# Kernel optimization log

Hardware: AMD Instinct MI355X
Metric: run time of the kernel (lower is better)

Reference implementation:

```python
import jax, jax.numpy as jnp
import numpy as np

EPS = 1e-5

def layer_norm(x, gamma, beta):
    mu = jnp.mean(x, axis=-1, keepdims=True)
    var = jnp.mean(jnp.square(x - mu), axis=-1, keepdims=True)
    return (x - mu) * jax.lax.rsqrt(var + EPS) * gamma + beta

def setup_inputs() -> dict:
    key = jax.random.key(0)
    ks = jax.random.split(key, 8)
    B, N, CZ, C = 1, 512, 128, 128
    s_z = 1.0 / np.sqrt(CZ)
    s_c = 1.0 / np.sqrt(C)
    return {
        "pair_rep": jax.random.normal(ks[0], (B, N, N, CZ), dtype=jnp.float32),
        "ln1_gamma": jnp.ones((CZ,), jnp.float32),
        "ln1_beta": jnp.zeros((CZ,), jnp.float32),
        "w_gate_a": jax.random.normal(ks[1], (CZ, C), jnp.float32) * s_z,
        "w_gate_b": jax.random.normal(ks[2], (CZ, C), jnp.float32) * s_z,
        "w_a": jax.random.normal(ks[3], (CZ, C), jnp.float32) * s_z,
        "w_b": jax.random.normal(ks[4], (CZ, C), jnp.float32) * s_z,
        "ln2_gamma": jnp.ones((C,), jnp.float32),
        "ln2_beta": jnp.zeros((C,), jnp.float32),
        "w_out": jax.random.normal(ks[5], (C, CZ), jnp.float32) * s_c,
        "w_gate": jax.random.normal(ks[6], (CZ, CZ), jnp.float32) * s_z,
    }

def reference(pair_rep, ln1_gamma, ln1_beta, w_gate_a, w_gate_b, w_a, w_b,
              ln2_gamma, ln2_beta, w_out, w_gate):
    # pair_rep: [B, N, N, CZ]
    z = layer_norm(pair_rep, ln1_gamma, ln1_beta)
    a = jax.nn.sigmoid(z @ w_gate_a) * (z @ w_a)   # [B, N, N, C]
    b = jax.nn.sigmoid(z @ w_gate_b) * (z @ w_b)   # [B, N, N, C]
    g = jax.nn.sigmoid(z @ w_gate)                 # [B, N, N, CZ]
    # triangle multiplicative update (outgoing): sum over third node k
    upd = jnp.einsum('bikc,bjkc->bijc', a, b)      # [B, N, N, C]
    upd = layer_norm(upd, ln2_gamma, ln2_beta) @ w_out  # [B, N, N, CZ]
    return g * upd
```

## Files before the change

### kernel.cpp

```cpp
#include <hip/hip_runtime.h>

#define N_ 512
#define NPOS (N_*N_)
#define CD 128

typedef unsigned short ushort_t;
typedef unsigned int   uint_t;
typedef __bf16 bf16_t;
typedef bf16_t  bf16x8 __attribute__((ext_vector_type(8)));
typedef float   f32x4  __attribute__((ext_vector_type(4)));
typedef unsigned short u16x4 __attribute__((ext_vector_type(4)));
typedef uint_t  u32x4 __attribute__((ext_vector_type(4)));

__device__ __forceinline__ float bf2f(ushort_t h) {
  union { uint_t u; float f; } v; v.u = ((uint_t)h) << 16; return v.f;
}
__device__ __forceinline__ ushort_t f2bf(float f) {
  union { float f; uint_t u; } v; v.f = f;
  uint_t u = v.u;
  return (ushort_t)((u + 0x7FFFu + ((u >> 16) & 1u)) >> 16);
}
__device__ __forceinline__ float sigm(float x) { return 1.0f / (1.0f + __expf(-x)); }

__global__ void k_tw(const float* s0, const float* s1, const float* s2,
                     const float* s3, const float* s4, const float* s5,
                     ushort_t* dst) {
  const float* s;
  switch (blockIdx.x) {
    case 0: s = s0; break; case 1: s = s1; break; case 2: s = s2; break;
    case 3: s = s3; break; case 4: s = s4; break; default: s = s5; break;
  }
  ushort_t* d = dst + blockIdx.x * CD * CD;
  for (int idx = threadIdx.x; idx < CD * CD; idx += 256) {
    int c = idx >> 7, k = idx & 127;
    d[idx] = f2bf(s[k * CD + c]);
  }
}

__global__ void k_ln1(const float* __restrict__ x, const float* __restrict__ gma,
                      const float* __restrict__ bta, ushort_t* __restrict__ z) {
  int row  = blockIdx.x * 4 + (threadIdx.x >> 6);
  int lane = threadIdx.x & 63;
  float2 pv = ((const float2*)(x + (size_t)row * CD))[lane];
  float x0 = pv.x, x1 = pv.y;
  float s = x0 + x1, q = x0 * x0 + x1 * x1;
  #pragma unroll
  for (int o = 32; o > 0; o >>= 1) { s += __shfl_xor(s, o, 64); q += __shfl_xor(q, o, 64); }
  float mu = s * (1.0f / 128.0f);
  float rs = rsqrtf(q * (1.0f / 128.0f) - mu * mu + 1e-5f);
  float2 gv = ((const float2*)gma)[lane];
  float2 bv = ((const float2*)bta)[lane];
  float z0 = (x0 - mu) * rs * gv.x + bv.x;
  float z1 = (x1 - mu) * rs * gv.y + bv.y;
  ((uint_t*)(z + (size_t)row * CD))[lane] = (uint_t)f2bf(z0) | ((uint_t)f2bf(z1) << 16);
}

__global__ __launch_bounds__(256, 1)
void k_proj(const ushort_t* __restrict__ z, const ushort_t* __restrict__ wT,
            ushort_t* __restrict__ aT, ushort_t* __restrict__ bT,
            float* __restrict__ g) {
  __shared__ ushort_t zl[128 * 128];
  __shared__ ushort_t tb[128][136];
  const int tid = threadIdx.x;
  const int lane = tid & 63, w = tid >> 6;
  const int qd = lane >> 4, l15 = lane & 15;

  bf16x8 wf[5][2][4];
  #pragma unroll
  for (int m = 0; m < 5; ++m)
    #pragma unroll
    for (int i = 0; i < 2; ++i)
      #pragma unroll
      for (int kk = 0; kk < 4; ++kk)
        wf[m][i][kk] = *(const bf16x8*)(wT + m * CD * CD + (w * 32 + i * 16 + l15) * CD + kk * 32 + qd * 8);

  const int TILES = 8;
  const int base = blockIdx.x * TILES;

  u32x4 st[8];
  {
    const u32x4* src = (const u32x4*)(z + (size_t)base * 128 * CD);
    #pragma unroll
    for (int i = 0; i < 8; ++i) st[i] = src[tid + i * 256];
  }

  for (int t = 0; t < TILES; ++t) {
    const int pos0 = (base + t) * 128;
    __syncthreads();
    {
      u32x4* dst = (u32x4*)zl;
      #pragma unroll
      for (int i = 0; i < 8; ++i) {
        int u = tid + i * 256, row = u >> 4;
        dst[(u & ~15) | ((u & 15) ^ (row & 7))] = st[i];
      }
    }
    __syncthreads();
    if (t + 1 < TILES) {
      const u32x4* src = (const u32x4*)(z + (size_t)(base + t + 1) * 128 * CD);
      #pragma unroll
      for (int i = 0; i < 8; ++i) st[i] = src[tid + i * 256];
    }

    #pragma unroll
    for (int ab = 0; ab < 2; ++ab) {
      f32x4 ag[2][8] = {}; f32x4 av[2][8] = {};
      #pragma unroll
      for (int kk = 0; kk < 4; ++kk) {
        bf16x8 zf[8];
        #pragma unroll
        for (int j = 0; j < 8; ++j) {
          int row = j * 16 + l15, kq = kk * 4 + qd;
          zf[j] = ((const bf16x8*)zl)[(row << 4) | (kq ^ (row & 7))];
        }
        #pragma unroll
        for (int j = 0; j < 8; ++j)
          #pragma unroll
          for (int i = 0; i < 2; ++i) {
            ag[i][j] = __builtin_amdgcn_mfma_f32_16x16x32_bf16(wf[ab * 2][i][kk],     zf[j], ag[i][j], 0, 0, 0);
            av[i][j] = __builtin_amdgcn_mfma_f32_16x16x32_bf16(wf[ab * 2 + 1][i][kk], zf[j], av[i][j], 0, 0, 0);
          }
      }
      #pragma unroll
      for (int i = 0; i < 2; ++i)
        #pragma unroll
        for (int j = 0; j < 8; ++j)
          #pragma unroll
          for (int r = 0; r < 4; ++r)
            tb[w * 32 + i * 16 + qd * 4 + r][j * 16 + l15] = f2bf(sigm(ag[i][j][r]) * av[i][j][r]);
      __syncthreads();
      {
        ushort_t* dst = ab ? bT : aT;
        #pragma unroll
        for (int it = 0; it < 8; ++it) {
          int idx = tid + it * 256;
          int row = idx >> 4, c16 = idx & 15;
          u32x4 v = *(const u32x4*)&tb[row][c16 * 8];
          *(u32x4*)&dst[(size_t)row * NPOS + pos0 + c16 * 8] = v;
        }
      }
      __syncthreads();
    }

    {
      f32x4 acc[2][8] = {};
      #pragma unroll
      for (int kk = 0; kk < 4; ++kk) {
        bf16x8 zf[8];
        #pragma unroll
        for (int j = 0; j < 8; ++j) {
          int row = j * 16 + l15, kq = kk * 4 + qd;
          zf[j] = ((const bf16x8*)zl)[(row << 4) | (kq ^ (row & 7))];
        }
        #pragma unroll
        for (int j = 0; j < 8; ++j)
          #pragma unroll
          for (int i = 0; i < 2; ++i)
            acc[i][j] = __builtin_amdgcn_mfma_f32_16x16x32_bf16(wf[4][i][kk], zf[j], acc[i][j], 0, 0, 0);
      }
      #pragma unroll
      for (int i = 0; i < 2; ++i) {
        int cz = w * 32 + i * 16 + qd * 4;
        #pragma unroll
        for (int j = 0; j < 8; ++j) {
          int pos = pos0 + j * 16 + l15;
          float4 pk;
          pk.x = sigm(acc[i][j][0]); pk.y = sigm(acc[i][j][1]);
          pk.z = sigm(acc[i][j][2]); pk.w = sigm(acc[i][j][3]);
          *(float4*)&g[(size_t)pos * CD + cz] = pk;
        }
      }
    }
  }
}

__global__ void k_tri(const ushort_t* __restrict__ aT, const ushort_t* __restrict__ bT,
                      ushort_t* __restrict__ uT) {
  __shared__ ushort_t lA[128][32];
  __shared__ ushort_t lB[128][32];
  __shared__ ushort_t tb[128][136];
  const int tid = threadIdx.x;
  const int lane = tid & 63, wid = tid >> 6;
  const int qd = lane >> 4, l15 = lane & 15;
  const int wm = wid & 1, wn = wid >> 1;
  const int c  = blockIdx.z;
  const int m0 = blockIdx.y * 128, n0 = blockIdx.x * 128;
  const ushort_t* A = aT + (size_t)c * NPOS;
  const ushort_t* B = bT + (size_t)c * NPOS;
  const int sr = tid >> 2, sc = (tid & 3) * 8;
  f32x4 acc[4][4] = {};
  for (int kk = 0; kk < N_; kk += 32) {
    __syncthreads();
    *(u32x4*)&lA[sr     ][sc] = *(const u32x4*)&A[(size_t)(m0 + sr)      * N_ + kk + sc];
    *(u32x4*)&lA[sr + 64][sc] = *(const u32x4*)&A[(size_t)(m0 + 64 + sr) * N_ + kk + sc];
    *(u32x4*)&lB[sr     ][sc] = *(const u32x4*)&B[(size_t)(n0 + sr)      * N_ + kk + sc];
    *(u32x4*)&lB[sr + 64][sc] = *(const u32x4*)&B[(size_t)(n0 + 64 + sr) * N_ + kk + sc];
    __syncthreads();
    bf16x8 af[4], bfr[4];
    #pragma unroll
    for (int t = 0; t < 4; ++t) af[t]  = *(const bf16x8*)&lA[wm * 64 + t * 16 + l15][qd * 8];
    #pragma unroll
    for (int t = 0; t < 4; ++t) bfr[t] = *(const bf16x8*)&lB[wn * 64 + t * 16 + l15][qd * 8];
    #pragma unroll
    for (int i = 0; i < 4; ++i)
      #pragma unroll
      for (int j = 0; j < 4; ++j)
        acc[i][j] = __builtin_amdgcn_mfma_f32_16x16x32_bf16(af[i], bfr[j], acc[i][j], 0, 0, 0);
  }
  #pragma unroll
  for (int i = 0; i < 4; ++i)
    #pragma unroll
    for (int j = 0; j < 4; ++j)
      #pragma unroll
      for (int r2 = 0; r2 < 4; ++r2)
        tb[wm * 64 + i * 16 + qd * 4 + r2][wn * 64 + j * 16 + l15] = f2bf(acc[i][j][r2]);
  __syncthreads();
  ushort_t* U = uT + (size_t)c * NPOS;
  #pragma unroll
  for (int it = 0; it < 8; ++it) {
    int idx = tid + it * 256;
    int row = idx >> 4, c16 = idx & 15;
    u32x4 v = *(const u32x4*)&tb[row][c16 * 8];
    *(u32x4*)&U[(size_t)(m0 + row) * N_ + n0 + c16 * 8] = v;
  }
}

__global__ void k_out(const ushort_t* __restrict__ uT, const ushort_t* __restrict__ wT,
                      const float* __restrict__ g2, const float* __restrict__ b2,
                      float* __restrict__ gout) {
  __shared__ ushort_t nu[128][136];
  __shared__ float ps[2][128], pq[2][128];
  __shared__ float mu[128], rsd[128], gam[128], bet[128];
  const int tid = threadIdx.x;
  const int lane = tid & 63, wid = tid >> 6;
  const int qd = lane >> 4, l15 = lane & 15;
  const int pos0 = blockIdx.x * 128;
  const ushort_t* WoT = wT + 5 * CD * CD;

  if (tid < 128) { gam[tid] = g2[tid]; bet[tid] = b2[tid]; }

  {
    int p = tid & 127, h = tid >> 7;
    float s = 0.f, sq = 0.f;
    for (int cc = h * 64; cc < h * 64 + 64; ++cc) {
      ushort_t raw = uT[(size_t)cc * NPOS + pos0 + p];
      nu[p][cc] = raw;
      float v = bf2f(raw); s += v; sq += v * v;
    }
    ps[h][p] = s; pq[h][p] = sq;
  }
  __syncthreads();
  if (tid < 128) {
    float s = ps[0][tid] + ps[1][tid];
    float m = s * (1.0f / 128.0f);
    float v = (pq[0][tid] + pq[1][tid]) * (1.0f / 128.0f) - m * m;
    mu[tid] = m; rsd[tid] = rsqrtf(v + 1e-5f);
  }
  __syncthreads();
  {
    int p = tid & 127, h = tid >> 7;
    float m = mu[p], rs = rsd[p];
    for (int cc = h * 64; cc < h * 64 + 64; ++cc)
      nu[p][cc] = f2bf((bf2f(nu[p][cc]) - m) * rs * gam[cc] + bet[cc]);
  }
  __syncthreads();

  const int wm = wid & 1, wn = wid >> 1;
  f32x4 acc[4][4] = {};
  for (int kk = 0; kk < 4; ++kk) {
    bf16x8 af[4];
    #pragma unroll
    for (int i = 0; i < 4; ++i)
      af[i] = *(const bf16x8*)(WoT + (wm * 64 + i * 16 + l15) * CD + kk * 32 + qd * 8);
    #pragma unroll
    for (int j = 0; j < 4; ++j) {
      bf16x8 bn = *(const bf16x8*)&nu[wn * 64 + j * 16 + l15][kk * 32 + qd * 8];
      #pragma unroll
      for (int i = 0; i < 4; ++i)
        acc[i][j] = __builtin_amdgcn_mfma_f32_16x16x32_bf16(af[i], bn, acc[i][j], 0, 0, 0);
    }
  }
  #pragma unroll
  for (int i = 0; i < 4; ++i) {
    int cz = wm * 64 + i * 16 + qd * 4;
    #pragma unroll
    for (int j = 0; j < 4; ++j) {
      int pos = pos0 + wn * 64 + j * 16 + l15;
      float4 gv = *(const float4*)&gout[(size_t)pos * CD + cz];
      float4 pk;
      pk.x = gv.x * acc[i][j][0]; pk.y = gv.y * acc[i][j][1];
      pk.z = gv.z * acc[i][j][2]; pk.w = gv.w * acc[i][j][3];
      *(float4*)&gout[(size_t)pos * CD + cz] = pk;
    }
  }
}

extern "C" void kernel_launch(void* const* d_in, const int* in_sizes, int n_in,
                              void* d_out, int out_size, void* d_ws, size_t ws_size,
                              hipStream_t stream) {
  const float* pair = (const float*)d_in[0];
  const float* g1   = (const float*)d_in[1];
  const float* b1   = (const float*)d_in[2];
  const float* wga  = (const float*)d_in[3];
  const float* wgb  = (const float*)d_in[4];
  const float* wa   = (const float*)d_in[5];
  const float* wb   = (const float*)d_in[6];
  const float* g2   = (const float*)d_in[7];
  const float* b2   = (const float*)d_in[8];
  const float* wout = (const float*)d_in[9];
  const float* wg   = (const float*)d_in[10];

  char* ws = (char*)d_ws;
  ushort_t* z  = (ushort_t*)(ws);
  ushort_t* aT = (ushort_t*)(ws + 67108864);
  ushort_t* bT = (ushort_t*)(ws + 134217728);
  ushort_t* wT = (ushort_t*)(ws + 201326592);
  ushort_t* uT = z;
  float*    gb = (float*)d_out;

  k_tw  <<<6, 256, 0, stream>>>(wga, wa, wgb, wb, wg, wout, wT);
  k_ln1 <<<NPOS / 4, 256, 0, stream>>>(pair, g1, b1, z);
  k_proj<<<256, 256, 0, stream>>>(z, wT, aT, bT, gb);
  k_tri <<<dim3(4, 4, 128), 256, 0, stream>>>(aT, bT, uT);
  k_out <<<2048, 256, 0, stream>>>(uT, wT, g2, b2, gb);
}
```

Before: 535.5 us.

## Fuse gate projection into output kernel, double-buffer triangle GEMM, vectorize LN1

The sigmoid gate projection moves from k_proj into k_out. k_out now recomputes LN1 from pair_rep for its 128 positions and runs a second MFMA GEMM against the gate weights alongside the output projection. This removes the 128MB fp32 gate write and its read back through the output buffer, at the cost of re-reading pair_rep and doing extra LDS work. k_tri gains a register-staged, double-buffered LDS pipeline with a swizzled layout, which cuts one barrier per k-step and avoids bank conflicts. k_ln1 is vectorized to 16 lanes per row with float4 loads, and k_proj uses fewer tiles per block with twice as many blocks.

```diff
diff --git a/kernel.cpp b/kernel.cpp
--- a/kernel.cpp
+++ b/kernel.cpp
@@ -39,42 +39,48 @@
 
 __global__ void k_ln1(const float* __restrict__ x, const float* __restrict__ gma,
                       const float* __restrict__ bta, ushort_t* __restrict__ z) {
-  int row  = blockIdx.x * 4 + (threadIdx.x >> 6);
-  int lane = threadIdx.x & 63;
-  float2 pv = ((const float2*)(x + (size_t)row * CD))[lane];
-  float x0 = pv.x, x1 = pv.y;
-  float s = x0 + x1, q = x0 * x0 + x1 * x1;
-  #pragma unroll
-  for (int o = 32; o > 0; o >>= 1) { s += __shfl_xor(s, o, 64); q += __shfl_xor(q, o, 64); }
+  const int tid  = threadIdx.x;
+  const int l15  = tid & 15;
+  const int row  = blockIdx.x * 16 + (tid >> 4);
+  const float4* src = (const float4*)(x + (size_t)row * CD + l15 * 8);
+  float4 v0 = src[0], v1 = src[1];
+  float s = ((v0.x + v0.y) + (v0.z + v0.w)) + ((v1.x + v1.y) + (v1.z + v1.w));
+  float q = ((v0.x*v0.x + v0.y*v0.y) + (v0.z*v0.z + v0.w*v0.w))
+          + ((v1.x*v1.x + v1.y*v1.y) + (v1.z*v1.z + v1.w*v1.w));
+  #pragma unroll
+  for (int o = 1; o < 16; o <<= 1) { s += __shfl_xor(s, o, 64); q += __shfl_xor(q, o, 64); }
   float mu = s * (1.0f / 128.0f);
   float rs = rsqrtf(q * (1.0f / 128.0f) - mu * mu + 1e-5f);
-  float2 gv = ((const float2*)gma)[lane];
-  float2 bv = ((const float2*)bta)[lane];
-  float z0 = (x0 - mu) * rs * gv.x + bv.x;
-  float z1 = (x1 - mu) * rs * gv.y + bv.y;
-  ((uint_t*)(z + (size_t)row * CD))[lane] = (uint_t)f2bf(z0) | ((uint_t)f2bf(z1) << 16);
+  const float4* gp = (const float4*)(gma + l15 * 8);
+  const float4* bp = (const float4*)(bta + l15 * 8);
+  float4 g0 = gp[0], g1v = gp[1], b0 = bp[0], b1v = bp[1];
+  uint_t w0 = (uint_t)f2bf((v0.x-mu)*rs*g0.x +b0.x ) | ((uint_t)f2bf((v0.y-mu)*rs*g0.y +b0.y ) << 16);
+  uint_t w1 = (uint_t)f2bf((v0.z-mu)*rs*g0.z +b0.z ) | ((uint_t)f2bf((v0.w-mu)*rs*g0.w +b0.w ) << 16);
+  uint_t w2 = (uint_t)f2bf((v1.x-mu)*rs*g1v.x+b1v.x) | ((uint_t)f2bf((v1.y-mu)*rs*g1v.y+b1v.y) << 16);
+  uint_t w3 = (uint_t)f2bf((v1.z-mu)*rs*g1v.z+b1v.z) | ((uint_t)f2bf((v1.w-mu)*rs*g1v.w+b1v.w) << 16);
+  u32x4 pk = {w0, w1, w2, w3};
+  *(u32x4*)(z + (size_t)row * CD + l15 * 8) = pk;
 }
 
 __global__ __launch_bounds__(256, 1)
 void k_proj(const ushort_t* __restrict__ z, const ushort_t* __restrict__ wT,
-            ushort_t* __restrict__ aT, ushort_t* __restrict__ bT,
-            float* __restrict__ g) {
+            ushort_t* __restrict__ aT, ushort_t* __restrict__ bT) {
   __shared__ ushort_t zl[128 * 128];
   __shared__ ushort_t tb[128][136];
   const int tid = threadIdx.x;
   const int lane = tid & 63, w = tid >> 6;
   const int qd = lane >> 4, l15 = lane & 15;
 
-  bf16x8 wf[5][2][4];
-  #pragma unroll
-  for (int m = 0; m < 5; ++m)
+  bf16x8 wf[4][2][4];
+  #pragma unroll
+  for (int m = 0; m < 4; ++m)
     #pragma unroll
     for (int i = 0; i < 2; ++i)
       #pragma unroll
       for (int kk = 0; kk < 4; ++kk)
         wf[m][i][kk] = *(const bf16x8*)(wT + m * CD * CD + (w * 32 + i * 16 + l15) * CD + kk * 32 + qd * 8);
 
-  const int TILES = 8;
+  const int TILES = 4;
   const int base = blockIdx.x * TILES;
 
   u32x4 st[8];
@@ -141,44 +147,16 @@
       }
       __syncthreads();
     }
-
-    {
-      f32x4 acc[2][8] = {};
-      #pragma unroll
-      for (int kk = 0; kk < 4; ++kk) {
-        bf16x8 zf[8];
-        #pragma unroll
-        for (int j = 0; j < 8; ++j) {
-          int row = j * 16 + l15, kq = kk * 4 + qd;
-          zf[j] = ((const bf16x8*)zl)[(row << 4) | (kq ^ (row & 7))];
-        }
-        #pragma unroll
-        for (int j = 0; j < 8; ++j)
-          #pragma unroll
-          for (int i = 0; i < 2; ++i)
-            acc[i][j] = __builtin_amdgcn_mfma_f32_16x16x32_bf16(wf[4][i][kk], zf[j], acc[i][j], 0, 0, 0);
-      }
-      #pragma unroll
-      for (int i = 0; i < 2; ++i) {
-        int cz = w * 32 + i * 16 + qd * 4;
-        #pragma unroll
-        for (int j = 0; j < 8; ++j) {
-          int pos = pos0 + j * 16 + l15;
-          float4 pk;
-          pk.x = sigm(acc[i][j][0]); pk.y = sigm(acc[i][j][1]);
-          pk.z = sigm(acc[i][j][2]); pk.w = sigm(acc[i][j][3]);
-          *(float4*)&g[(size_t)pos * CD + cz] = pk;
-        }
-      }
-    }
-  }
-}
-
+  }
+}
+
+__device__ __forceinline__ int uofs(int row, int c4) {
+  return (row * 4 + (c4 ^ ((row >> 1) & 3))) * 8;
+}
 __global__ void k_tri(const ushort_t* __restrict__ aT, const ushort_t* __restrict__ bT,
                       ushort_t* __restrict__ uT) {
-  __shared__ ushort_t lA[128][32];
-  __shared__ ushort_t lB[128][32];
-  __shared__ ushort_t tb[128][136];
+  __shared__ u32x4 smem4[2176];
+  ushort_t* lds = (ushort_t*)smem4;
   const int tid = threadIdx.x;
   const int lane = tid & 63, wid = tid >> 6;
   const int qd = lane >> 4, l15 = lane & 15;
@@ -187,26 +165,50 @@
   const int m0 = blockIdx.y * 128, n0 = blockIdx.x * 128;
   const ushort_t* A = aT + (size_t)c * NPOS;
   const ushort_t* B = bT + (size_t)c * NPOS;
-  const int sr = tid >> 2, sc = (tid & 3) * 8;
+  const int sr = tid >> 2, c4 = tid & 3;
+
+  u32x4 rA0, rA1, rB0, rB1;
+  rA0 = *(const u32x4*)&A[(size_t)(m0 + sr)      * N_ + c4 * 8];
+  rA1 = *(const u32x4*)&A[(size_t)(m0 + 64 + sr) * N_ + c4 * 8];
+  rB0 = *(const u32x4*)&B[(size_t)(n0 + sr)      * N_ + c4 * 8];
+  rB1 = *(const u32x4*)&B[(size_t)(n0 + 64 + sr) * N_ + c4 * 8];
+  *(u32x4*)&lds[       uofs(sr,      c4)] = rA0;
+  *(u32x4*)&lds[       uofs(sr + 64, c4)] = rA1;
+  *(u32x4*)&lds[8192 + uofs(sr,      c4)] = rB0;
+  *(u32x4*)&lds[8192 + uofs(sr + 64, c4)] = rB1;
+
   f32x4 acc[4][4] = {};
-  for (int kk = 0; kk < N_; kk += 32) {
+  for (int it = 1; it <= 16; ++it) {
     __syncthreads();
-    *(u32x4*)&lA[sr     ][sc] = *(const u32x4*)&A[(size_t)(m0 + sr)      * N_ + kk + sc];
-    *(u32x4*)&lA[sr + 64][sc] = *(const u32x4*)&A[(size_t)(m0 + 64 + sr) * N_ + kk + sc];
-    *(u32x4*)&lB[sr     ][sc] = *(const u32x4*)&B[(size_t)(n0 + sr)      * N_ + kk + sc];
-    *(u32x4*)&lB[sr + 64][sc] = *(const u32x4*)&B[(size_t)(n0 + 64 + sr) * N_ + kk + sc];
-    __syncthreads();
+    const int curb = (it - 1) & 1, nxt = it & 1;
+    if (it < 16) {
+      const int ko = it * 32;
+      rA0 = *(const u32x4*)&A[(size_t)(m0 + sr)      * N_ + ko + c4 * 8];
+      rA1 = *(const u32x4*)&A[(size_t)(m0 + 64 + sr) * N_ + ko + c4 * 8];
+      rB0 = *(const u32x4*)&B[(size_t)(n0 + sr)      * N_ + ko + c4 * 8];
+      rB1 = *(const u32x4*)&B[(size_t)(n0 + 64 + sr) * N_ + ko + c4 * 8];
+    }
+    const ushort_t* la = lds + curb * 4096;
+    const ushort_t* lb = lds + 8192 + curb * 4096;
     bf16x8 af[4], bfr[4];
     #pragma unroll
-    for (int t = 0; t < 4; ++t) af[t]  = *(const bf16x8*)&lA[wm * 64 + t * 16 + l15][qd * 8];
-    #pragma unroll
-    for (int t = 0; t < 4; ++t) bfr[t] = *(const bf16x8*)&lB[wn * 64 + t * 16 + l15][qd * 8];
+    for (int t = 0; t < 4; ++t) af[t]  = *(const bf16x8*)&la[uofs(wm * 64 + t * 16 + l15, qd)];
+    #pragma unroll
+    for (int t = 0; t < 4; ++t) bfr[t] = *(const bf16x8*)&lb[uofs(wn * 64 + t * 16 + l15, qd)];
     #pragma unroll
     for (int i = 0; i < 4; ++i)
       #pragma unroll
       for (int j = 0; j < 4; ++j)
         acc[i][j] = __builtin_amdgcn_mfma_f32_16x16x32_bf16(af[i], bfr[j], acc[i][j], 0, 0, 0);
-  }
+    if (it < 16) {
+      *(u32x4*)&lds[nxt * 4096 +        uofs(sr,      c4)] = rA0;
+      *(u32x4*)&lds[nxt * 4096 +        uofs(sr + 64, c4)] = rA1;
+      *(u32x4*)&lds[8192 + nxt * 4096 + uofs(sr,      c4)] = rB0;
+      *(u32x4*)&lds[8192 + nxt * 4096 + uofs(sr + 64, c4)] = rB1;
+    }
+  }
+  __syncthreads();
+  ushort_t (*tb)[136] = (ushort_t(*)[136])smem4;
   #pragma unroll
   for (int i = 0; i < 4; ++i)
     #pragma unroll
@@ -225,19 +227,65 @@
   }
 }
 
-__global__ void k_out(const ushort_t* __restrict__ uT, const ushort_t* __restrict__ wT,
-                      const float* __restrict__ g2, const float* __restrict__ b2,
-                      float* __restrict__ gout) {
+__global__ __launch_bounds__(256, 2)
+void k_out(const ushort_t* __restrict__ uT, const ushort_t* __restrict__ wT,
+           const float* __restrict__ pair,
+           const float* __restrict__ g1, const float* __restrict__ b1,
+           const float* __restrict__ g2, const float* __restrict__ b2,
+           float* __restrict__ gout) {
   __shared__ ushort_t nu[128][136];
+  __shared__ ushort_t zn[128][136];
   __shared__ float ps[2][128], pq[2][128];
   __shared__ float mu[128], rsd[128], gam[128], bet[128];
   const int tid = threadIdx.x;
   const int lane = tid & 63, wid = tid >> 6;
   const int qd = lane >> 4, l15 = lane & 15;
   const int pos0 = blockIdx.x * 128;
+  const ushort_t* WgT = wT + 4 * CD * CD;
   const ushort_t* WoT = wT + 5 * CD * CD;
 
   if (tid < 128) { gam[tid] = g2[tid]; bet[tid] = b2[tid]; }
+
+  {
+    int r = tid >> 1, h = tid & 1;
+    const float4* src = (const float4*)(pair + (size_t)(pos0 + r) * CD + h * 64);
+    float s = 0.f, sq = 0.f;
+    #pragma unroll
+    for (int u = 0; u < 16; ++u) {
+      float4 v = src[u];
+      s  += (v.x + v.y) + (v.z + v.w);
+      sq += (v.x*v.x + v.y*v.y) + (v.z*v.z + v.w*v.w);
+    }
+    ps[h][r] = s; pq[h][r] = sq;
+  }
+  __syncthreads();
+  if (tid < 128) {
+    float s = ps[0][tid] + ps[1][tid];
+    float m = s * (1.0f / 128.0f);
+    float v = (pq[0][tid] + pq[1][tid]) * (1.0f / 128.0f) - m * m;
+    mu[tid] = m; rsd[tid] = rsqrtf(v + 1e-5f);
+  }
+  __syncthreads();
+  {
+    int r = tid >> 1, h = tid & 1;
+    float m = mu[r], rs = rsd[r];
+    const float4* src = (const float4*)(pair + (size_t)(pos0 + r) * CD + h * 64);
+    const float4* gp = (const float4*)(g1 + h * 64);
+    const float4* bp = (const float4*)(b1 + h * 64);
+    #pragma unroll
+    for (int u2 = 0; u2 < 8; ++u2) {
+      float4 v0 = src[u2*2], v1 = src[u2*2+1];
+      float4 ga = gp[u2*2], gb2 = gp[u2*2+1];
+      float4 ba = bp[u2*2], bb2 = bp[u2*2+1];
+      uint_t w0 = (uint_t)f2bf((v0.x-m)*rs*ga.x +ba.x ) | ((uint_t)f2bf((v0.y-m)*rs*ga.y +ba.y ) << 16);
+      uint_t w1 = (uint_t)f2bf((v0.z-m)*rs*ga.z +ba.z ) | ((uint_t)f2bf((v0.w-m)*rs*ga.w +ba.w ) << 16);
+      uint_t w2 = (uint_t)f2bf((v1.x-m)*rs*gb2.x+bb2.x) | ((uint_t)f2bf((v1.y-m)*rs*gb2.y+bb2.y) << 16);
+      uint_t w3 = (uint_t)f2bf((v1.z-m)*rs*gb2.z+bb2.z) | ((uint_t)f2bf((v1.w-m)*rs*gb2.w+bb2.w) << 16);
+      u32x4 pk = {w0, w1, w2, w3};
+      *(u32x4*)&zn[r][h * 64 + u2 * 8] = pk;
+    }
+  }
+  __syncthreads();
 
   {
     int p = tid & 127, h = tid >> 7;
@@ -266,18 +314,24 @@
   __syncthreads();
 
   const int wm = wid & 1, wn = wid >> 1;
-  f32x4 acc[4][4] = {};
+  f32x4 ao[4][4] = {}; f32x4 agt[4][4] = {};
   for (int kk = 0; kk < 4; ++kk) {
-    bf16x8 af[4];
-    #pragma unroll
-    for (int i = 0; i < 4; ++i)
-      af[i] = *(const bf16x8*)(WoT + (wm * 64 + i * 16 + l15) * CD + kk * 32 + qd * 8);
+    bf16x8 afo[4], afg[4];
+    #pragma unroll
+    for (int i = 0; i < 4; ++i) {
+      int wrow = (wm * 64 + i * 16 + l15) * CD + kk * 32 + qd * 8;
+      afo[i] = *(const bf16x8*)(WoT + wrow);
+      afg[i] = *(const bf16x8*)(WgT + wrow);
+    }
     #pragma unroll
     for (int j = 0; j < 4; ++j) {
       bf16x8 bn = *(const bf16x8*)&nu[wn * 64 + j * 16 + l15][kk * 32 + qd * 8];
-      #pragma unroll
-      for (int i = 0; i < 4; ++i)
-        acc[i][j] = __builtin_amdgcn_mfma_f32_16x16x32_bf16(af[i], bn, acc[i][j], 0, 0, 0);
+      bf16x8 bz = *(const bf16x8*)&zn[wn * 64 + j * 16 + l15][kk * 32 + qd * 8];
+      #pragma unroll
+      for (int i = 0; i < 4; ++i) {
+        ao[i][j]  = __builtin_amdgcn_mfma_f32_16x16x32_bf16(afo[i], bn, ao[i][j],  0, 0, 0);
+        agt[i][j] = __builtin_amdgcn_mfma_f32_16x16x32_bf16(afg[i], bz, agt[i][j], 0, 0, 0);
+      }
     }
   }
   #pragma unroll
@@ -286,10 +340,11 @@
     #pragma unroll
     for (int j = 0; j < 4; ++j) {
       int pos = pos0 + wn * 64 + j * 16 + l15;
-      float4 gv = *(const float4*)&gout[(size_t)pos * CD + cz];
       float4 pk;
-      pk.x = gv.x * acc[i][j][0]; pk.y = gv.y * acc[i][j][1];
-      pk.z = gv.z * acc[i][j][2]; pk.w = gv.w * acc[i][j][3];
+      pk.x = sigm(agt[i][j][0]) * ao[i][j][0];
+      pk.y = sigm(agt[i][j][1]) * ao[i][j][1];
+      pk.z = sigm(agt[i][j][2]) * ao[i][j][2];
+      pk.w = sigm(agt[i][j][3]) * ao[i][j][3];
       *(float4*)&gout[(size_t)pos * CD + cz] = pk;
     }
   }
@@ -319,8 +374,8 @@
   float*    gb = (float*)d_out;
 
   k_tw  <<<6, 256, 0, stream>>>(wga, wa, wgb, wb, wg, wout, wT);
-  k_ln1 <<<NPOS / 4, 256, 0, stream>>>(pair, g1, b1, z);
-  k_proj<<<256, 256, 0, stream>>>(z, wT, aT, bT, gb);
+  k_ln1 <<<NPOS / 16, 256, 0, stream>>>(pair, g1, b1, z);
+  k_proj<<<512, 256, 0, stream>>>(z, wT, aT, bT);
   k_tri <<<dim3(4, 4, 128), 256, 0, stream>>>(aT, bT, uT);
-  k_out <<<2048, 256, 0, stream>>>(uT, wT, g2, b2, gb);
-}
+  k_out <<<2048, 256, 0, stream>>>(uT, wT, pair, g1, b1, g2, b2, gb);
+}
```

New measurement: 547.0 us. +2.2%, slower.
